# Kernel tuning notes

Hardware: AMD Instinct MI355X
Metric: run time of the kernel (lower is better)

## Reference

```python
import jax, jax.numpy as jnp
import numpy as np

N, D, E, K = 8192, 256, 262144, 8


def _linear_params(key, fan_in, fan_out):
    kw, kb = jax.random.split(key)
    s = 1.0 / np.sqrt(fan_in)
    W = jax.random.uniform(kw, (fan_in, fan_out), jnp.float32, -s, s)
    b = jax.random.uniform(kb, (fan_out,), jnp.float32, -s, s)
    return W, b


def setup_inputs() -> dict:
    key = jax.random.key(0)
    ks = jax.random.split(key, 8)
    enc = jax.random.normal(ks[0], (N, D), jnp.float32)
    edge_index = jax.random.randint(ks[1], (2, E), 0, N, jnp.int64)
    edge_attr = jax.random.uniform(ks[2], (E,), jnp.float32)
    ADJ = jax.random.bernoulli(ks[3], 32.0 / N, (N, N)).astype(jnp.float32)
    eps = jax.random.normal(ks[4], (N, K, D), jnp.float32)  # randn_like noise
    W1, b1 = _linear_params(ks[5], 2 * D, D)
    W2, b2 = _linear_params(ks[6], 2 * D, D)
    W3, b3 = _linear_params(ks[7], D, D)
    W4, b4 = _linear_params(jax.random.fold_in(key, 99), D, D)
    return dict(enc=enc, edge_index=edge_index, edge_attr=edge_attr, ADJ=ADJ,
                eps=eps, W1=W1, b1=b1, W2=W2, b2=b2, W3=W3, b3=b3, W4=W4, b4=b4)


def _simple_conv_cat(x, src, dst, w):
    # PyG SimpleConv(aggr='mean', combine_root='cat'):
    # weighted messages from src, mean-aggregated at dst, concat [root, agg]
    msg = x[src] * w[:, None]                                   # [E, D]
    agg = jax.ops.segment_sum(msg, dst, num_segments=N)         # [N, D]
    cnt = jax.ops.segment_sum(jnp.ones_like(w), dst, num_segments=N)
    agg = agg / jnp.maximum(cnt, 1.0)[:, None]
    return jnp.concatenate([x, agg], axis=-1)                   # [N, 2D]


def reference(enc, edge_index, edge_attr, ADJ, eps, W1, b1, W2, b2, W3, b3, W4, b4):
    src, dst = edge_index[0], edge_index[1]  # flow: source -> target
    # GNN: two SimpleConv + Linear + ReLU blocks
    h = _simple_conv_cat(enc, src, dst, edge_attr)
    h = jax.nn.relu(h @ W1 + b1)
    h = _simple_conv_cat(h, src, dst, edge_attr)
    h = jax.nn.relu(h @ W2 + b2)
    enc2 = h + enc
    mu = (enc2 @ W3 + b3)[:, None, :]                            # [N,1,D] -> broadcast K
    log_var = (enc2 @ W4 + b4)[:, None, :]
    mu = jnp.broadcast_to(mu, (N, K, D))
    log_var = jnp.broadcast_to(log_var, (N, K, D))
    Z = mu + eps * jnp.exp(0.5 * log_var)                        # [N,K,D]
    kl = -0.5 * jnp.mean(jnp.sum(1.0 + log_var - mu ** 2 - jnp.exp(log_var), axis=-1))
    Z_l = Z.mean(axis=1)                                         # [N,D]
    logits = Z_l @ Z_l.T                                         # [N,N]
    graph_loss = jnp.mean(jax.nn.softplus(logits) - logits * ADJ)  # BCEWithLogits
    vae_loss = kl + graph_loss
    return enc2, Z, vae_loss
```

## Files before the change

### kernel.cpp

```cpp
#include <hip/hip_runtime.h>

#define NN 8192
#define DD 256
#define EE 262144

typedef __attribute__((ext_vector_type(8))) short bf16x8;
typedef __attribute__((ext_vector_type(4))) float f32x4;

static __device__ __forceinline__ unsigned short f2b(float x) {
  unsigned int u = __float_as_uint(x);
  u += 0x7fffu + ((u >> 16) & 1u);
  return (unsigned short)(u >> 16);
}
static __device__ __forceinline__ float b2f(unsigned short u) {
  return __uint_as_float(((unsigned int)u) << 16);
}

__global__ void k_count(const int* __restrict__ dst, int* __restrict__ cnt) {
  int e = blockIdx.x * 256 + threadIdx.x;
  if (e < EE) atomicAdd(&cnt[dst[e]], 1);
}

__global__ void k_scan(const int* __restrict__ cnt, int* __restrict__ row_ptr) {
  __shared__ int s[1024];
  int t = threadIdx.x;
  int loc[8]; int tot = 0;
#pragma unroll
  for (int i = 0; i < 8; ++i) { loc[i] = cnt[t * 8 + i]; tot += loc[i]; }
  s[t] = tot; __syncthreads();
  for (int off = 1; off < 1024; off <<= 1) {
    int v = s[t];
    int add = (t >= off) ? s[t - off] : 0;
    __syncthreads();
    s[t] = v + add;
    __syncthreads();
  }
  int run = (t == 0) ? 0 : s[t - 1];
#pragma unroll
  for (int i = 0; i < 8; ++i) { row_ptr[t * 8 + i] = run; run += loc[i]; }
  if (t == 1023) row_ptr[NN] = run;
}

__global__ void k_fill(const int* __restrict__ dst, const int* __restrict__ src,
                       const float* __restrict__ w, const int* __restrict__ row_ptr,
                       int* __restrict__ fill, int* __restrict__ slist,
                       float* __restrict__ wlist) {
  int e = blockIdx.x * 256 + threadIdx.x;
  if (e < EE) {
    int d = dst[e];
    int idx = atomicAdd(&fill[d], 1);
    int pos = row_ptr[d] + idx;
    slist[pos] = src[e];
    wlist[pos] = w[e];
  }
}

__global__ __launch_bounds__(256) void k_conv(const unsigned short* __restrict__ xb,
                                              const int* __restrict__ slist,
                                              const float* __restrict__ wlist,
                                              const int* __restrict__ row_ptr,
                                              unsigned short* __restrict__ out) {
  int tid = threadIdx.x, wid = tid >> 6, lane = tid & 63;
  int n = blockIdx.x * 4 + wid;
  const ushort4* x4 = (const ushort4*)xb;
  float ax = 0.f, ay = 0.f, az = 0.f, aw = 0.f;
  int b = row_ptr[n], e2 = row_ptr[n + 1];
  int i = b;
  for (; i + 1 < e2; i += 2) {
    int s0 = slist[i], s1 = slist[i + 1];
    float w0 = wlist[i], w1 = wlist[i + 1];
    ushort4 v0 = x4[(size_t)s0 * 64 + lane];
    ushort4 v1 = x4[(size_t)s1 * 64 + lane];
    ax += b2f(v0.x) * w0 + b2f(v1.x) * w1;
    ay += b2f(v0.y) * w0 + b2f(v1.y) * w1;
    az += b2f(v0.z) * w0 + b2f(v1.z) * w1;
    aw += b2f(v0.w) * w0 + b2f(v1.w) * w1;
  }
  if (i < e2) {
    int s0 = slist[i];
    float w0 = wlist[i];
    ushort4 v0 = x4[(size_t)s0 * 64 + lane];
    ax += b2f(v0.x) * w0; ay += b2f(v0.y) * w0;
    az += b2f(v0.z) * w0; aw += b2f(v0.w) * w0;
  }
  float inv = 1.0f / fmaxf((float)(e2 - b), 1.0f);
  ushort4 rv = x4[(size_t)n * 64 + lane];
  ushort4 av;
  av.x = f2b(ax * inv); av.y = f2b(ay * inv);
  av.z = f2b(az * inv); av.w = f2b(aw * inv);
  *(ushort4*)&out[(size_t)n * 512 + lane * 4]       = rv;
  *(ushort4*)&out[(size_t)n * 512 + 256 + lane * 4] = av;
}

static __device__ __forceinline__ void gemm_core(const unsigned short* __restrict__ A,
                                                 const unsigned short* __restrict__ BT,
                                                 int K, int m0, int n0,
                                                 unsigned short* As, unsigned short* Bs,
                                                 f32x4 acc[4][4]) {
  const int tid = threadIdx.x;
  const int lane = tid & 63, wid = tid >> 6;
  const int wr = wid >> 1, wc = wid & 1;
  const int r16 = lane & 15, g = lane >> 4;
  for (int kt = 0; kt < K; kt += 64) {
    __syncthreads();
#pragma unroll
    for (int j = 0; j < 4; ++j) {
      int c = tid + j * 256;
      int row = c >> 3, slot = c & 7;
      int sw = (slot ^ (row & 7)) << 3;
      *(bf16x8*)&As[row * 64 + sw] = *(const bf16x8*)&A[(size_t)(m0 + row) * K + kt + slot * 8];
      *(bf16x8*)&Bs[row * 64 + sw] = *(const bf16x8*)&BT[(size_t)(n0 + row) * K + kt + slot * 8];
    }
    __syncthreads();
#pragma unroll
    for (int kk = 0; kk < 64; kk += 32) {
      bf16x8 av[4], bv[4];
      int bslot = (kk >> 3) + g;
#pragma unroll
      for (int m = 0; m < 4; ++m) {
        int row = wr * 64 + m * 16 + r16;
        av[m] = *(const bf16x8*)&As[row * 64 + ((bslot ^ (row & 7)) << 3)];
      }
#pragma unroll
      for (int n2 = 0; n2 < 4; ++n2) {
        int row = wc * 64 + n2 * 16 + r16;
        bv[n2] = *(const bf16x8*)&Bs[row * 64 + ((bslot ^ (row & 7)) << 3)];
      }
#pragma unroll
      for (int m = 0; m < 4; ++m)
#pragma unroll
        for (int n2 = 0; n2 < 4; ++n2)
          acc[m][n2] = __builtin_amdgcn_mfma_f32_16x16x32_bf16(av[m], bv[n2], acc[m][n2], 0, 0, 0);
    }
  }
}

template <bool RELU, bool RESID, bool WC, bool WB>
__global__ __launch_bounds__(256) void k_gemm(const unsigned short* __restrict__ A,
                                              const unsigned short* __restrict__ BT,
                                              const float* __restrict__ bias,
                                              const float* __restrict__ resid,
                                              float* __restrict__ C,
                                              unsigned short* __restrict__ Cb,
                                              int K, int Ncols) {
  __shared__ unsigned short As[128 * 64];
  __shared__ unsigned short Bs[128 * 64];
  f32x4 acc[4][4] = {};
  int m0 = blockIdx.x * 128, n0 = blockIdx.y * 128;
  gemm_core(A, BT, K, m0, n0, As, Bs, acc);
  const int tid = threadIdx.x;
  const int lane = tid & 63, wid = tid >> 6;
  const int wr = wid >> 1, wc = wid & 1;
  const int r16 = lane & 15, g = lane >> 4;
#pragma unroll
  for (int m = 0; m < 4; ++m)
#pragma unroll
    for (int rr = 0; rr < 4; ++rr) {
      int grow = m0 + wr * 64 + m * 16 + g * 4 + rr;
#pragma unroll
      for (int n2 = 0; n2 < 4; ++n2) {
        int gcol = n0 + wc * 64 + n2 * 16 + r16;
        float v = acc[m][n2][rr] + bias[gcol];
        if (RELU) v = fmaxf(v, 0.f);
        if (RESID) v += resid[(size_t)grow * Ncols + gcol];
        if (WC) C[(size_t)grow * Ncols + gcol] = v;
        if (WB) Cb[(size_t)grow * Ncols + gcol] = f2b(v);
      }
    }
}

__global__ __launch_bounds__(256) void k_logits(const unsigned short* __restrict__ Zl,
                                                double* __restrict__ sp_sum) {
  int bx = blockIdx.x, by = blockIdx.y;
  if (by < bx) return;
  __shared__ unsigned short As[128 * 64];
  __shared__ unsigned short Bs[128 * 64];
  f32x4 acc[4][4] = {};
  int m0 = bx * 128, n0 = by * 128;
  gemm_core(Zl, Zl, 256, m0, n0, As, Bs, acc);
  const int tid = threadIdx.x;
  float wgt = (bx == by) ? 1.0f : 2.0f;
  float lsum = 0.f;
#pragma unroll
  for (int m = 0; m < 4; ++m)
#pragma unroll
    for (int rr = 0; rr < 4; ++rr)
#pragma unroll
      for (int n2 = 0; n2 < 4; ++n2) {
        float c = acc[m][n2][rr];
        lsum += fmaxf(c, 0.f) + __logf(1.0f + __expf(-fabsf(c)));
      }
  lsum *= wgt;
  __syncthreads();
  float* red = (float*)As;
  red[tid] = lsum;
  __syncthreads();
  for (int off = 128; off > 0; off >>= 1) {
    if (tid < off) red[tid] += red[tid + off];
    __syncthreads();
  }
  if (tid == 0) atomicAdd(sp_sum, (double)red[0]);
}

__global__ __launch_bounds__(256) void k_adj(const float* __restrict__ ADJ,
                                             const unsigned short* __restrict__ Zl,
                                             double* __restrict__ dot_sum) {
  int tid = threadIdx.x, wid = tid >> 6, lane = tid & 63;
  int i = blockIdx.x * 4 + wid;
  const ushort4* z4 = (const ushort4*)Zl;
  ushort4 ziv = z4[(size_t)i * 64 + lane];
  float zx = b2f(ziv.x), zy = b2f(ziv.y), zz = b2f(ziv.z), zw = b2f(ziv.w);
  float sx = 0.f, sy = 0.f, sz = 0.f, sw = 0.f;
  const float4* a4 = (const float4*)(ADJ + (size_t)i * NN);
#pragma unroll 1
  for (int c0 = 0; c0 < 32; ++c0) {
    float4 a = a4[c0 * 64 + lane];
    bool any = (a.x != 0.f) | (a.y != 0.f) | (a.z != 0.f) | (a.w != 0.f);
    unsigned long long m = __ballot(any);
    while (m) {
      int l = __ffsll((long long)m) - 1;
      m &= m - 1;
      float axx = __shfl(a.x, l), ayy = __shfl(a.y, l);
      float azz = __shfl(a.z, l), aww = __shfl(a.w, l);
      int jb = c0 * 256 + l * 4;
      if (axx != 0.f) {
        ushort4 v = z4[(size_t)(jb + 0) * 64 + lane];
        sx += axx * b2f(v.x); sy += axx * b2f(v.y); sz += axx * b2f(v.z); sw += axx * b2f(v.w);
      }
      if (ayy != 0.f) {
        ushort4 v = z4[(size_t)(jb + 1) * 64 + lane];
        sx += ayy * b2f(v.x); sy += ayy * b2f(v.y); sz += ayy * b2f(v.z); sw += ayy * b2f(v.w);
      }
      if (azz != 0.f) {
        ushort4 v = z4[(size_t)(jb + 2) * 64 + lane];
        sx += azz * b2f(v.x); sy += azz * b2f(v.y); sz += azz * b2f(v.z); sw += azz * b2f(v.w);
      }
      if (aww != 0.f) {
        ushort4 v = z4[(size_t)(jb + 3) * 64 + lane];
        sx += aww * b2f(v.x); sy += aww * b2f(v.y); sz += aww * b2f(v.z); sw += aww * b2f(v.w);
      }
    }
  }
  float t = zx * sx + zy * sy + zz * sz + zw * sw;
#pragma unroll
  for (int off = 32; off > 0; off >>= 1) t += __shfl_down(t, off, 64);
  __shared__ float red[4];
  if (lane == 0) red[wid] = t;
  __syncthreads();
  if (tid == 0) atomicAdd(dot_sum, (double)(red[0] + red[1] + red[2] + red[3]));
}

__global__ __launch_bounds__(256) void k_z(const float* __restrict__ mulv,
                                           const float* __restrict__ eps,
                                           float* __restrict__ Zout,
                                           unsigned short* __restrict__ Zl,
                                           double* __restrict__ kl_sum) {
  int tid = threadIdx.x, wid = tid >> 6, lane = tid & 63;
  int n = blockIdx.x * 4 + wid;
  const float4* m4 = (const float4*)mulv;
  float4 mu = m4[(size_t)n * 128 + lane];
  float4 lv = m4[(size_t)n * 128 + 64 + lane];
  float4 sig;
  sig.x = __expf(0.5f * lv.x); sig.y = __expf(0.5f * lv.y);
  sig.z = __expf(0.5f * lv.z); sig.w = __expf(0.5f * lv.w);
  const float4* e4 = (const float4*)eps;
  float4* z4 = (float4*)Zout;
  float esx = 0.f, esy = 0.f, esz = 0.f, esw = 0.f;
#pragma unroll
  for (int k = 0; k < 8; ++k) {
    size_t idx = ((size_t)n * 8 + k) * 64 + lane;
    float4 e = e4[idx];
    float4 z;
    z.x = mu.x + e.x * sig.x; z.y = mu.y + e.y * sig.y;
    z.z = mu.z + e.z * sig.z; z.w = mu.w + e.w * sig.w;
    z4[idx] = z;
    esx += e.x; esy += e.y; esz += e.z; esw += e.w;
  }
  ushort4 zl;
  zl.x = f2b(mu.x + sig.x * esx * 0.125f);
  zl.y = f2b(mu.y + sig.y * esy * 0.125f);
  zl.z = f2b(mu.z + sig.z * esz * 0.125f);
  zl.w = f2b(mu.w + sig.w * esw * 0.125f);
  *(ushort4*)&Zl[(size_t)n * 256 + lane * 4] = zl;
  float t = (1.0f + lv.x - mu.x * mu.x - sig.x * sig.x)
          + (1.0f + lv.y - mu.y * mu.y - sig.y * sig.y)
          + (1.0f + lv.z - mu.z * mu.z - sig.z * sig.z)
          + (1.0f + lv.w - mu.w * mu.w - sig.w * sig.w);
#pragma unroll
  for (int off = 32; off > 0; off >>= 1) t += __shfl_down(t, off, 64);
  __shared__ float red[4];
  if (lane == 0) red[wid] = t;
  __syncthreads();
  if (tid == 0) atomicAdd(kl_sum, (double)(red[0] + red[1] + red[2] + red[3]));
}

__global__ void k_prep(const float* __restrict__ enc,
                       const float* __restrict__ W1, const float* __restrict__ W2,
                       const float* __restrict__ W3, const float* __restrict__ W4,
                       const float* __restrict__ b3, const float* __restrict__ b4,
                       unsigned short* __restrict__ encb,
                       unsigned short* __restrict__ W1t, unsigned short* __restrict__ W2t,
                       unsigned short* __restrict__ W34t, float* __restrict__ b34) {
  int idx = blockIdx.x * 256 + threadIdx.x;
  {
    float4 v = ((const float4*)enc)[idx];
    ushort4 o;
    o.x = f2b(v.x); o.y = f2b(v.y); o.z = f2b(v.z); o.w = f2b(v.w);
    ((ushort4*)encb)[idx] = o;
  }
  if (idx < 512 * 256) {
    int k = idx >> 8, n = idx & 255;
    W1t[n * 512 + k] = f2b(W1[idx]);
    W2t[n * 512 + k] = f2b(W2[idx]);
  }
  if (idx < 256 * 512) {
    int k = idx >> 9, n = idx & 511;
    float v = (n < 256) ? W3[k * 256 + n] : W4[k * 256 + (n - 256)];
    W34t[n * 256 + k] = f2b(v);
  }
  if (idx < 512) b34[idx] = (idx < 256) ? b3[idx] : b4[idx - 256];
}

__global__ void k_final(const double* __restrict__ sums, float* __restrict__ out) {
  double kl = -0.5 * sums[0] / (double)NN;
  double gl = (sums[1] - sums[2]) / ((double)NN * (double)NN);
  out[0] = (float)(kl + gl);
}

extern "C" void kernel_launch(void* const* d_in, const int* in_sizes, int n_in,
                              void* d_out, int out_size, void* d_ws, size_t ws_size,
                              hipStream_t stream) {
  const float* enc = (const float*)d_in[0];
  const int*   ei  = (const int*)d_in[1];
  const int*   src = ei;
  const int*   dst = ei + EE;
  const float* w   = (const float*)d_in[2];
  const float* ADJ = (const float*)d_in[3];
  const float* eps = (const float*)d_in[4];
  const float* W1  = (const float*)d_in[5];
  const float* b1  = (const float*)d_in[6];
  const float* W2  = (const float*)d_in[7];
  const float* b2  = (const float*)d_in[8];
  const float* W3  = (const float*)d_in[9];
  const float* b3  = (const float*)d_in[10];
  const float* W4  = (const float*)d_in[11];
  const float* b4  = (const float*)d_in[12];

  char* ws = (char*)d_ws;
  size_t off = 0;
  auto alloc = [&](size_t bytes) -> void* {
    void* p = ws + off;
    off = (off + bytes + 255) & ~(size_t)255;
    return p;
  };
  unsigned short* h1b   = (unsigned short*)alloc((size_t)NN * 512 * 2);
  unsigned short* hb    = (unsigned short*)alloc((size_t)NN * 256 * 2);
  float*          mulv  = (float*)alloc((size_t)NN * 512 * 4);
  unsigned short* enc2b = (unsigned short*)alloc((size_t)NN * 256 * 2);
  unsigned short* Zlb   = (unsigned short*)alloc((size_t)NN * 256 * 2);
  unsigned short* encb  = (unsigned short*)alloc((size_t)NN * 256 * 2);
  unsigned short* W1t   = (unsigned short*)alloc(512 * 256 * 2);
  unsigned short* W2t   = (unsigned short*)alloc(512 * 256 * 2);
  unsigned short* W34t  = (unsigned short*)alloc(512 * 256 * 2);
  float*          b34v  = (float*)alloc(512 * 4);
  int*            cnt   = (int*)alloc(NN * 4);
  int*            row_ptr = (int*)alloc((NN + 1) * 4);
  int*            fill  = (int*)alloc(NN * 4);
  int*            slist = (int*)alloc((size_t)EE * 4);
  float*          wlist = (float*)alloc((size_t)EE * 4);
  double*         sums  = (double*)alloc(32);

  float* out_enc2 = (float*)d_out;
  float* out_Z    = out_enc2 + (size_t)NN * 256;
  float* out_loss = out_Z + (size_t)NN * 8 * 256;

  hipMemsetAsync(cnt, 0, NN * 4, stream);
  hipMemsetAsync(fill, 0, NN * 4, stream);
  hipMemsetAsync(sums, 0, 32, stream);

  k_prep<<<2048, 256, 0, stream>>>(enc, W1, W2, W3, W4, b3, b4, encb, W1t, W2t, W34t, b34v);
  k_count<<<EE / 256, 256, 0, stream>>>(dst, cnt);
  k_scan<<<1, 1024, 0, stream>>>(cnt, row_ptr);
  k_fill<<<EE / 256, 256, 0, stream>>>(dst, src, w, row_ptr, fill, slist, wlist);

  k_conv<<<NN / 4, 256, 0, stream>>>(encb, slist, wlist, row_ptr, h1b);
  k_gemm<true, false, false, true><<<dim3(64, 2), 256, 0, stream>>>(h1b, W1t, b1, nullptr, nullptr, hb, 512, 256);
  k_conv<<<NN / 4, 256, 0, stream>>>(hb, slist, wlist, row_ptr, h1b);
  k_gemm<true, true, true, true><<<dim3(64, 2), 256, 0, stream>>>(h1b, W2t, b2, enc, out_enc2, enc2b, 512, 256);
  k_gemm<false, false, true, false><<<dim3(64, 4), 256, 0, stream>>>(enc2b, W34t, b34v, nullptr, mulv, nullptr, 256, 512);
  k_z<<<NN / 4, 256, 0, stream>>>(mulv, eps, out_Z, Zlb, sums);
  k_adj<<<NN / 4, 256, 0, stream>>>(ADJ, Zlb, sums + 2);
  k_logits<<<dim3(64, 64), 256, 0, stream>>>(Zlb, sums + 1);
  k_final<<<1, 1, 0, stream>>>(sums, out_loss);
}
```

Before: 659.0 us.

## Fuse logits, ADJ-dot and final loss into one kernel with ticket finalization

Merges the logits GEMM-softplus reduction, the sparse ADJ dot-product pass and the scalar loss finalization into a single launch, with blockIdx.y selecting the role. The last block to finish, found with an atomic ticket, computes the loss, replacing the separate single-thread kernel. The intent is to overlap the memory-bound ADJ scan with the compute-bound logits tiles and to cut launch overhead. The three memsets move into the prep kernel, and ADJ loads are paired two per iteration. The cost is a more fragile block count (NBLK_TOTAL must match the blocks that do not exit early) and heavier resource use in the combined kernel.

```diff
diff --git a/kernel.cpp b/kernel.cpp
--- a/kernel.cpp
+++ b/kernel.cpp
@@ -14,6 +14,39 @@
 }
 static __device__ __forceinline__ float b2f(unsigned short u) {
   return __uint_as_float(((unsigned int)u) << 16);
+}
+
+__global__ void k_prep(const float* __restrict__ enc,
+                       const float* __restrict__ W1, const float* __restrict__ W2,
+                       const float* __restrict__ W3, const float* __restrict__ W4,
+                       const float* __restrict__ b3, const float* __restrict__ b4,
+                       unsigned short* __restrict__ encb,
+                       unsigned short* __restrict__ W1t, unsigned short* __restrict__ W2t,
+                       unsigned short* __restrict__ W34t, float* __restrict__ b34,
+                       int* __restrict__ cnt, int* __restrict__ fill,
+                       double* __restrict__ sums, int* __restrict__ ticket) {
+  int idx = blockIdx.x * 256 + threadIdx.x;
+  {
+    float4 v = ((const float4*)enc)[idx];
+    ushort4 o;
+    o.x = f2b(v.x); o.y = f2b(v.y); o.z = f2b(v.z); o.w = f2b(v.w);
+    ((ushort4*)encb)[idx] = o;
+  }
+  if (idx < 512 * 256) {
+    int k = idx >> 8, n = idx & 255;
+    W1t[n * 512 + k] = f2b(W1[idx]);
+    W2t[n * 512 + k] = f2b(W2[idx]);
+  }
+  if (idx < 256 * 512) {
+    int k = idx >> 9, n = idx & 511;
+    float v = (n < 256) ? W3[k * 256 + n] : W4[k * 256 + (n - 256)];
+    W34t[n * 256 + k] = f2b(v);
+  }
+  if (idx < 512) b34[idx] = (idx < 256) ? b3[idx] : b4[idx - 256];
+  if (idx < NN) cnt[idx] = 0;
+  else if (idx < 2 * NN) fill[idx - NN] = 0;
+  else if (idx < 2 * NN + 4) sums[idx - 2 * NN] = 0.0;
+  else if (idx == 2 * NN + 4) *ticket = 0;
 }
 
 __global__ void k_count(const int* __restrict__ dst, int* __restrict__ cnt) {
@@ -169,87 +202,6 @@
     }
 }
 
-__global__ __launch_bounds__(256) void k_logits(const unsigned short* __restrict__ Zl,
-                                                double* __restrict__ sp_sum) {
-  int bx = blockIdx.x, by = blockIdx.y;
-  if (by < bx) return;
-  __shared__ unsigned short As[128 * 64];
-  __shared__ unsigned short Bs[128 * 64];
-  f32x4 acc[4][4] = {};
-  int m0 = bx * 128, n0 = by * 128;
-  gemm_core(Zl, Zl, 256, m0, n0, As, Bs, acc);
-  const int tid = threadIdx.x;
-  float wgt = (bx == by) ? 1.0f : 2.0f;
-  float lsum = 0.f;
-#pragma unroll
-  for (int m = 0; m < 4; ++m)
-#pragma unroll
-    for (int rr = 0; rr < 4; ++rr)
-#pragma unroll
-      for (int n2 = 0; n2 < 4; ++n2) {
-        float c = acc[m][n2][rr];
-        lsum += fmaxf(c, 0.f) + __logf(1.0f + __expf(-fabsf(c)));
-      }
-  lsum *= wgt;
-  __syncthreads();
-  float* red = (float*)As;
-  red[tid] = lsum;
-  __syncthreads();
-  for (int off = 128; off > 0; off >>= 1) {
-    if (tid < off) red[tid] += red[tid + off];
-    __syncthreads();
-  }
-  if (tid == 0) atomicAdd(sp_sum, (double)red[0]);
-}
-
-__global__ __launch_bounds__(256) void k_adj(const float* __restrict__ ADJ,
-                                             const unsigned short* __restrict__ Zl,
-                                             double* __restrict__ dot_sum) {
-  int tid = threadIdx.x, wid = tid >> 6, lane = tid & 63;
-  int i = blockIdx.x * 4 + wid;
-  const ushort4* z4 = (const ushort4*)Zl;
-  ushort4 ziv = z4[(size_t)i * 64 + lane];
-  float zx = b2f(ziv.x), zy = b2f(ziv.y), zz = b2f(ziv.z), zw = b2f(ziv.w);
-  float sx = 0.f, sy = 0.f, sz = 0.f, sw = 0.f;
-  const float4* a4 = (const float4*)(ADJ + (size_t)i * NN);
-#pragma unroll 1
-  for (int c0 = 0; c0 < 32; ++c0) {
-    float4 a = a4[c0 * 64 + lane];
-    bool any = (a.x != 0.f) | (a.y != 0.f) | (a.z != 0.f) | (a.w != 0.f);
-    unsigned long long m = __ballot(any);
-    while (m) {
-      int l = __ffsll((long long)m) - 1;
-      m &= m - 1;
-      float axx = __shfl(a.x, l), ayy = __shfl(a.y, l);
-      float azz = __shfl(a.z, l), aww = __shfl(a.w, l);
-      int jb = c0 * 256 + l * 4;
-      if (axx != 0.f) {
-        ushort4 v = z4[(size_t)(jb + 0) * 64 + lane];
-        sx += axx * b2f(v.x); sy += axx * b2f(v.y); sz += axx * b2f(v.z); sw += axx * b2f(v.w);
-      }
-      if (ayy != 0.f) {
-        ushort4 v = z4[(size_t)(jb + 1) * 64 + lane];
-        sx += ayy * b2f(v.x); sy += ayy * b2f(v.y); sz += ayy * b2f(v.z); sw += ayy * b2f(v.w);
-      }
-      if (azz != 0.f) {
-        ushort4 v = z4[(size_t)(jb + 2) * 64 + lane];
-        sx += azz * b2f(v.x); sy += azz * b2f(v.y); sz += azz * b2f(v.z); sw += azz * b2f(v.w);
-      }
-      if (aww != 0.f) {
-        ushort4 v = z4[(size_t)(jb + 3) * 64 + lane];
-        sx += aww * b2f(v.x); sy += aww * b2f(v.y); sz += aww * b2f(v.z); sw += aww * b2f(v.w);
-      }
-    }
-  }
-  float t = zx * sx + zy * sy + zz * sz + zw * sw;
-#pragma unroll
-  for (int off = 32; off > 0; off >>= 1) t += __shfl_down(t, off, 64);
-  __shared__ float red[4];
-  if (lane == 0) red[wid] = t;
-  __syncthreads();
-  if (tid == 0) atomicAdd(dot_sum, (double)(red[0] + red[1] + red[2] + red[3]));
-}
-
 __global__ __launch_bounds__(256) void k_z(const float* __restrict__ mulv,
                                            const float* __restrict__ eps,
                                            float* __restrict__ Zout,
@@ -294,37 +246,105 @@
   if (tid == 0) atomicAdd(kl_sum, (double)(red[0] + red[1] + red[2] + red[3]));
 }
 
-__global__ void k_prep(const float* __restrict__ enc,
-                       const float* __restrict__ W1, const float* __restrict__ W2,
-                       const float* __restrict__ W3, const float* __restrict__ W4,
-                       const float* __restrict__ b3, const float* __restrict__ b4,
-                       unsigned short* __restrict__ encb,
-                       unsigned short* __restrict__ W1t, unsigned short* __restrict__ W2t,
-                       unsigned short* __restrict__ W34t, float* __restrict__ b34) {
-  int idx = blockIdx.x * 256 + threadIdx.x;
-  {
-    float4 v = ((const float4*)enc)[idx];
-    ushort4 o;
-    o.x = f2b(v.x); o.y = f2b(v.y); o.z = f2b(v.z); o.w = f2b(v.w);
-    ((ushort4*)encb)[idx] = o;
-  }
-  if (idx < 512 * 256) {
-    int k = idx >> 8, n = idx & 255;
-    W1t[n * 512 + k] = f2b(W1[idx]);
-    W2t[n * 512 + k] = f2b(W2[idx]);
-  }
-  if (idx < 256 * 512) {
-    int k = idx >> 9, n = idx & 511;
-    float v = (n < 256) ? W3[k * 256 + n] : W4[k * 256 + (n - 256)];
-    W34t[n * 256 + k] = f2b(v);
-  }
-  if (idx < 512) b34[idx] = (idx < 256) ? b3[idx] : b4[idx - 256];
-}
-
-__global__ void k_final(const double* __restrict__ sums, float* __restrict__ out) {
-  double kl = -0.5 * sums[0] / (double)NN;
-  double gl = (sums[1] - sums[2]) / ((double)NN * (double)NN);
-  out[0] = (float)(kl + gl);
+#define NBLK_TOTAL (2080 + 2048)
+__global__ __launch_bounds__(256) void k_loss(const unsigned short* __restrict__ Zl,
+                                              const float* __restrict__ ADJ,
+                                              double* __restrict__ sums,
+                                              int* __restrict__ ticket,
+                                              float* __restrict__ out_loss) {
+  __shared__ unsigned short As[128 * 64];
+  __shared__ unsigned short Bs[128 * 64];
+  const int bx = blockIdx.x, by = blockIdx.y;
+  const int tid = threadIdx.x, wid = tid >> 6, lane = tid & 63;
+
+  if (by < 64) {
+    if (by < bx) return;
+    f32x4 acc[4][4] = {};
+    gemm_core(Zl, Zl, 256, bx * 128, by * 128, As, Bs, acc);
+    float lsum = 0.f;
+#pragma unroll
+    for (int m = 0; m < 4; ++m)
+#pragma unroll
+      for (int rr = 0; rr < 4; ++rr)
+#pragma unroll
+        for (int n2 = 0; n2 < 4; ++n2) {
+          float c = acc[m][n2][rr];
+          lsum += fmaxf(c, 0.f) + __logf(1.0f + __expf(-fabsf(c)));
+        }
+    lsum *= (bx == by) ? 1.0f : 2.0f;
+    __syncthreads();
+    float* red = (float*)As;
+    red[tid] = lsum;
+    __syncthreads();
+    for (int off = 128; off > 0; off >>= 1) {
+      if (tid < off) red[tid] += red[tid + off];
+      __syncthreads();
+    }
+    if (tid == 0) atomicAdd(&sums[1], (double)red[0]);
+  } else {
+    int r = (by - 64) * 64 + bx;
+    int i = r * 4 + wid;
+    const ushort4* z4 = (const ushort4*)Zl;
+    ushort4 ziv = z4[(size_t)i * 64 + lane];
+    float zx = b2f(ziv.x), zy = b2f(ziv.y), zz = b2f(ziv.z), zw = b2f(ziv.w);
+    float sx = 0.f, sy = 0.f, sz = 0.f, sw = 0.f;
+    const float4* a4 = (const float4*)(ADJ + (size_t)i * NN);
+#pragma unroll 1
+    for (int c0 = 0; c0 < 32; c0 += 2) {
+      float4 a0 = a4[(c0 + 0) * 64 + lane];
+      float4 a1 = a4[(c0 + 1) * 64 + lane];
+#pragma unroll
+      for (int u = 0; u < 2; ++u) {
+        float4 a = u ? a1 : a0;
+        int cc = c0 + u;
+        bool any = (a.x != 0.f) | (a.y != 0.f) | (a.z != 0.f) | (a.w != 0.f);
+        unsigned long long m = __ballot(any);
+        while (m) {
+          int l = __ffsll((long long)m) - 1;
+          m &= m - 1;
+          float axx = __shfl(a.x, l), ayy = __shfl(a.y, l);
+          float azz = __shfl(a.z, l), aww = __shfl(a.w, l);
+          int jb = cc * 256 + l * 4;
+          if (axx != 0.f) {
+            ushort4 v = z4[(size_t)(jb + 0) * 64 + lane];
+            sx += axx * b2f(v.x); sy += axx * b2f(v.y); sz += axx * b2f(v.z); sw += axx * b2f(v.w);
+          }
+          if (ayy != 0.f) {
+            ushort4 v = z4[(size_t)(jb + 1) * 64 + lane];
+            sx += ayy * b2f(v.x); sy += ayy * b2f(v.y); sz += ayy * b2f(v.z); sw += ayy * b2f(v.w);
+          }
+          if (azz != 0.f) {
+            ushort4 v = z4[(size_t)(jb + 2) * 64 + lane];
+            sx += azz * b2f(v.x); sy += azz * b2f(v.y); sz += azz * b2f(v.z); sw += azz * b2f(v.w);
+          }
+          if (aww != 0.f) {
+            ushort4 v = z4[(size_t)(jb + 3) * 64 + lane];
+            sx += aww * b2f(v.x); sy += aww * b2f(v.y); sz += aww * b2f(v.z); sw += aww * b2f(v.w);
+          }
+        }
+      }
+    }
+    float t = zx * sx + zy * sy + zz * sz + zw * sw;
+#pragma unroll
+    for (int off = 32; off > 0; off >>= 1) t += __shfl_down(t, off, 64);
+    __shared__ float red2[4];
+    if (lane == 0) red2[wid] = t;
+    __syncthreads();
+    if (tid == 0) atomicAdd(&sums[2], (double)(red2[0] + red2[1] + red2[2] + red2[3]));
+  }
+
+  if (tid == 0) {
+    __threadfence();
+    int old = atomicAdd(ticket, 1);
+    if (old == NBLK_TOTAL - 1) {
+      double kl_s  = atomicAdd(&sums[0], 0.0);
+      double sp_s  = atomicAdd(&sums[1], 0.0);
+      double dot_s = atomicAdd(&sums[2], 0.0);
+      double kl = -0.5 * kl_s / (double)NN;
+      double gl = (sp_s - dot_s) / ((double)NN * (double)NN);
+      out_loss[0] = (float)(kl + gl);
+    }
+  }
 }
 
 extern "C" void kernel_launch(void* const* d_in, const int* in_sizes, int n_in,
@@ -369,16 +389,14 @@
   int*            slist = (int*)alloc((size_t)EE * 4);
   float*          wlist = (float*)alloc((size_t)EE * 4);
   double*         sums  = (double*)alloc(32);
+  int*            ticket = (int*)alloc(16);
 
   float* out_enc2 = (float*)d_out;
   float* out_Z    = out_enc2 + (size_t)NN * 256;
   float* out_loss = out_Z + (size_t)NN * 8 * 256;
 
-  hipMemsetAsync(cnt, 0, NN * 4, stream);
-  hipMemsetAsync(fill, 0, NN * 4, stream);
-  hipMemsetAsync(sums, 0, 32, stream);
-
-  k_prep<<<2048, 256, 0, stream>>>(enc, W1, W2, W3, W4, b3, b4, encb, W1t, W2t, W34t, b34v);
+  k_prep<<<2048, 256, 0, stream>>>(enc, W1, W2, W3, W4, b3, b4, encb, W1t, W2t, W34t,
+                                   b34v, cnt, fill, sums, ticket);
   k_count<<<EE / 256, 256, 0, stream>>>(dst, cnt);
   k_scan<<<1, 1024, 0, stream>>>(cnt, row_ptr);
   k_fill<<<EE / 256, 256, 0, stream>>>(dst, src, w, row_ptr, fill, slist, wlist);
@@ -389,7 +407,5 @@
   k_gemm<true, true, true, true><<<dim3(64, 2), 256, 0, stream>>>(h1b, W2t, b2, enc, out_enc2, enc2b, 512, 256);
   k_gemm<false, false, true, false><<<dim3(64, 4), 256, 0, stream>>>(enc2b, W34t, b34v, nullptr, mulv, nullptr, 256, 512);
   k_z<<<NN / 4, 256, 0, stream>>>(mulv, eps, out_Z, Zlb, sums);
-  k_adj<<<NN / 4, 256, 0, stream>>>(ADJ, Zlb, sums + 2);
-  k_logits<<<dim3(64, 64), 256, 0, stream>>>(Zlb, sums + 1);
-  k_final<<<1, 1, 0, stream>>>(sums, out_loss);
-}
+  k_loss<<<dim3(64, 96), 256, 0, stream>>>(Zlb, ADJ, sums, ticket, out_loss);
+}
```

New measurement: 779.2 us. +18.2%, slower.
